# Performance work log

Hardware: AMD Instinct MI355X
Metric: run time of the kernel (lower is better)

Reference implementation:

```python
import jax, jax.numpy as jnp
import numpy as np


def setup_inputs() -> dict:
    key = jax.random.key(0)
    ks = jax.random.split(key, 7)
    B = 65536
    x = jax.random.normal(ks[0], (B, 1, 28, 28), dtype=jnp.float32)
    conv_w = jax.random.normal(ks[1], (4, 1, 7, 7), dtype=jnp.float32) * 0.1
    conv_b = jax.random.normal(ks[2], (4,), dtype=jnp.float32) * 0.1
    fc1_w = jax.random.normal(ks[3], (64, 256), dtype=jnp.float32) * 0.05
    fc1_b = jax.random.normal(ks[4], (64,), dtype=jnp.float32) * 0.05
    fc2_w = jax.random.normal(ks[5], (10, 64), dtype=jnp.float32) * 0.1
    fc2_b = jax.random.normal(ks[6], (10,), dtype=jnp.float32) * 0.1
    return {"x": x, "conv_w": conv_w, "conv_b": conv_b,
            "fc1_w": fc1_w, "fc1_b": fc1_b, "fc2_w": fc2_w, "fc2_b": fc2_b}


def reference(x, conv_w, conv_b, fc1_w, fc1_b, fc2_w, fc2_b):
    # conv1: 1->4 channels, 7x7 kernel, stride 3, no padding -> [B,4,8,8]
    h = jax.lax.conv_general_dilated(
        x, conv_w, window_strides=(3, 3), padding="VALID",
        dimension_numbers=("NCHW", "OIHW", "NCHW"))
    h = h + conv_b[None, :, None, None]
    h = h * h  # SquareFunction (CKKS polynomial activation)
    h = h.reshape(h.shape[0], -1)  # [B, 256]
    h = jnp.einsum("bi,oi->bo", h, fc1_w) + fc1_b
    h = h * h  # SquareFunction
    out = jnp.einsum("bi,oi->bo", h, fc2_w) + fc2_b  # [B, 10]
    return out
```

## Files before the change

### kernel.cpp

```cpp
#include <hip/hip_runtime.h>


#define BLK_IMGS    32
#define CHUNK_IMGS  8
#define NCHUNK      4
#define XCH_FLOATS  (CHUNK_IMGS * 784)
#define HB_PITCH    33
#define H2_PITCH    33

#define LDS_XBUF    0
#define LDS_H       6272
#define LDS_H2      14720
#define LDS_W2      16832
#define LDS_OUT     17856
#define LDS_TOTAL_F 18176

__global__ __launch_bounds__(512)
void encconv_fused8(const float* __restrict__ x,
                    const float* __restrict__ conv_w,
                    const float* __restrict__ conv_b,
                    const float* __restrict__ fc1_w,
                    const float* __restrict__ fc1_b,
                    const float* __restrict__ fc2_w,
                    const float* __restrict__ fc2_b,
                    float* __restrict__ out)
{
    extern __shared__ float lds[];
    float*  xbuf = lds + LDS_XBUF;
    float4* hb   = (float4*)(lds + LDS_H);
    float4* h2b  = (float4*)(lds + LDS_H2);
    float4* w2b  = (float4*)(lds + LDS_W2);
    float*  ob   = lds + LDS_OUT;

    const int tid  = threadIdx.x;
    const int blk  = blockIdx.x;
    const long base_img = (long)blk * BLK_IMGS;

    const int lane = tid & 63;
    const int wv   = tid >> 6;

    const int c    = __builtin_amdgcn_readfirstlane(wv >> 1);
    const int ghi  = __builtin_amdgcn_readfirstlane(wv & 1);
    const int glo  = lane >> 4;
    const int y    = (lane >> 1) & 7;
    const int xh   = lane & 1;
    const int g    = ghi * 4 + glo;

    float ws[49];
    #pragma unroll
    for (int i = 0; i < 49; ++i) ws[i] = conv_w[c * 49 + i];
    const float cb = conv_b[c];

    if (tid < 160) {
        float4 v = *(const float4*)(fc2_w + tid * 4);
        int e  = tid * 4;
        int j  = e >> 6;
        int kk = (e & 63) >> 2;
        w2b[kk * 16 + j] = v;
    }

    const float* xblk = x + base_img * 784;

    float4 pf0, pf1, pf2, pf3;
    {
        const float* src = xblk;
        pf0 = *(const float4*)(src + 4 * tid);
        pf1 = *(const float4*)(src + 4 * (tid + 512));
        pf2 = *(const float4*)(src + 4 * (tid + 1024));
        if (tid < 32) pf3 = *(const float4*)(src + 4 * (tid + 1536));
    }

    for (int ch = 0; ch < NCHUNK; ++ch) {
        *(float4*)(xbuf + 4 * tid)          = pf0;
        *(float4*)(xbuf + 4 * (tid + 512))  = pf1;
        *(float4*)(xbuf + 4 * (tid + 1024)) = pf2;
        if (tid < 32) *(float4*)(xbuf + 4 * (tid + 1536)) = pf3;
        __syncthreads();

        if (ch + 1 < NCHUNK) {
            const float* src = xblk + (ch + 1) * XCH_FLOATS;
            pf0 = *(const float4*)(src + 4 * tid);
            pf1 = *(const float4*)(src + 4 * (tid + 512));
            pf2 = *(const float4*)(src + 4 * (tid + 1024));
            if (tid < 32) pf3 = *(const float4*)(src + 4 * (tid + 1536));
        }

        float acc0 = 0.f, acc1 = 0.f, acc2 = 0.f, acc3 = 0.f;
        const float* xi = xbuf + g * 784;
        #pragma unroll
        for (int rr = 0; rr < 7; ++rr) {
            const float* rp = xi + (3 * y + rr) * 28 + 12 * xh;
            float4 r0 = *(const float4*)(rp + 0);
            float4 r1 = *(const float4*)(rp + 4);
            float4 r2 = *(const float4*)(rp + 8);
            float4 r3 = *(const float4*)(rp + 12);
            float r[16] = { r0.x, r0.y, r0.z, r0.w,
                            r1.x, r1.y, r1.z, r1.w,
                            r2.x, r2.y, r2.z, r2.w,
                            r3.x, r3.y, r3.z, r3.w };
            #pragma unroll
            for (int kx = 0; kx < 7; ++kx) {
                const float w = ws[rr * 7 + kx];
                acc0 = fmaf(r[0 + kx], w, acc0);
                acc1 = fmaf(r[3 + kx], w, acc1);
                acc2 = fmaf(r[6 + kx], w, acc2);
                acc3 = fmaf(r[9 + kx], w, acc3);
            }
        }

        float4 hv;
        hv.x = acc0 + cb; hv.x *= hv.x;
        hv.y = acc1 + cb; hv.y *= hv.y;
        hv.z = acc2 + cb; hv.z *= hv.z;
        hv.w = acc3 + cb; hv.w *= hv.w;
        hb[(c * 16 + y * 2 + xh) * HB_PITCH + (ch * CHUNK_IMGS + g)] = hv;

        __syncthreads();
    }

    {
        const int img = lane & 31;
        const int oh  = lane >> 5;
        const int w8  = __builtin_amdgcn_readfirstlane(wv);
        const float* wbase = fc1_w + (w8 * 8) * 256;

        float a0=0.f,a1=0.f,a2=0.f,a3=0.f,a4=0.f,a5=0.f,a6=0.f,a7=0.f;

        #pragma unroll 2
        for (int k4 = 0; k4 < 64; ++k4) {
            float4 h4 = hb[k4 * HB_PITCH + img];
            const float* wp = wbase + k4 * 4;
            float4 w0 = *(const float4*)(wp + 0 * 256);
            float4 w1 = *(const float4*)(wp + 1 * 256);
            float4 w2 = *(const float4*)(wp + 2 * 256);
            float4 w3 = *(const float4*)(wp + 3 * 256);
            float4 w4 = *(const float4*)(wp + 4 * 256);
            float4 w5 = *(const float4*)(wp + 5 * 256);
            float4 w6 = *(const float4*)(wp + 6 * 256);
            float4 w7 = *(const float4*)(wp + 7 * 256);
            a0 = fmaf(h4.x,w0.x,a0); a0 = fmaf(h4.y,w0.y,a0); a0 = fmaf(h4.z,w0.z,a0); a0 = fmaf(h4.w,w0.w,a0);
            a1 = fmaf(h4.x,w1.x,a1); a1 = fmaf(h4.y,w1.y,a1); a1 = fmaf(h4.z,w1.z,a1); a1 = fmaf(h4.w,w1.w,a1);
            a2 = fmaf(h4.x,w2.x,a2); a2 = fmaf(h4.y,w2.y,a2); a2 = fmaf(h4.z,w2.z,a2); a2 = fmaf(h4.w,w2.w,a2);
            a3 = fmaf(h4.x,w3.x,a3); a3 = fmaf(h4.y,w3.y,a3); a3 = fmaf(h4.z,w3.z,a3); a3 = fmaf(h4.w,w3.w,a3);
            a4 = fmaf(h4.x,w4.x,a4); a4 = fmaf(h4.y,w4.y,a4); a4 = fmaf(h4.z,w4.z,a4); a4 = fmaf(h4.w,w4.w,a4);
            a5 = fmaf(h4.x,w5.x,a5); a5 = fmaf(h4.y,w5.y,a5); a5 = fmaf(h4.z,w5.z,a5); a5 = fmaf(h4.w,w5.w,a5);
            a6 = fmaf(h4.x,w6.x,a6); a6 = fmaf(h4.y,w6.y,a6); a6 = fmaf(h4.z,w6.z,a6); a6 = fmaf(h4.w,w6.w,a6);
            a7 = fmaf(h4.x,w7.x,a7); a7 = fmaf(h4.y,w7.y,a7); a7 = fmaf(h4.z,w7.z,a7); a7 = fmaf(h4.w,w7.w,a7);
        }

        const float* bp = fc1_b + w8 * 8;
        float s0 = oh ? a4 : a0;  float b0 = oh ? bp[4] : bp[0];
        float s1 = oh ? a5 : a1;  float b1 = oh ? bp[5] : bp[1];
        float s2 = oh ? a6 : a2;  float b2 = oh ? bp[6] : bp[2];
        float s3 = oh ? a7 : a3;  float b3 = oh ? bp[7] : bp[3];
        float4 p0;
        p0.x = s0 + b0; p0.x *= p0.x;
        p0.y = s1 + b1; p0.y *= p0.y;
        p0.z = s2 + b2; p0.z *= p0.z;
        p0.w = s3 + b3; p0.w *= p0.w;
        h2b[(w8 * 2 + oh) * H2_PITCH + img] = p0;
    }
    __syncthreads();

    {
        const int im5 = tid >> 4;
        const int q   = tid & 15;
        if (q < 10) {
            float s = 0.f;
            #pragma unroll
            for (int k4 = 0; k4 < 16; ++k4) {
                float4 hh = h2b[k4 * H2_PITCH + im5];
                float4 wA = w2b[k4 * 16 + q];
                s = fmaf(hh.x, wA.x, s); s = fmaf(hh.y, wA.y, s);
                s = fmaf(hh.z, wA.z, s); s = fmaf(hh.w, wA.w, s);
            }
            ob[im5 * 10 + q] = s + fc2_b[q];
        }
    }
    __syncthreads();

    if (tid < 80) {
        float4 v = *(const float4*)(ob + tid * 4);
        *(float4*)(out + (long)blk * 320 + tid * 4) = v;
    }
}

extern "C" void kernel_launch(void* const* d_in, const int* in_sizes, int n_in,
                              void* d_out, int out_size, void* d_ws, size_t ws_size,
                              hipStream_t stream) {
    const float* x      = (const float*)d_in[0];
    const float* conv_w = (const float*)d_in[1];
    const float* conv_b = (const float*)d_in[2];
    const float* fc1_w  = (const float*)d_in[3];
    const float* fc1_b  = (const float*)d_in[4];
    const float* fc2_w  = (const float*)d_in[5];
    const float* fc2_b  = (const float*)d_in[6];
    float* out = (float*)d_out;

    const int B = in_sizes[0] / 784;
    const int blocks = (B + BLK_IMGS - 1) / BLK_IMGS;
    const size_t lds_bytes = LDS_TOTAL_F * sizeof(float);

    static bool attr_set = false;
    if (!attr_set) {
        (void)hipFuncSetAttribute((const void*)encconv_fused8,
                                  hipFuncAttributeMaxDynamicSharedMemorySize,
                                  (int)lds_bytes);
        attr_set = true;
    }

    encconv_fused8<<<blocks, 512, lds_bytes, stream>>>(
        x, conv_w, conv_b, fc1_w, fc1_b, fc2_w, fc2_b, out);
}
```

Baseline: 344.2 us.

## Halve conv chunk size and alias LDS buffers to shrink footprint

```diff
diff --git a/kernel.cpp b/kernel.cpp
--- a/kernel.cpp
+++ b/kernel.cpp
@@ -2,21 +2,19 @@
 
 
 #define BLK_IMGS    32
-#define CHUNK_IMGS  8
-#define NCHUNK      4
+#define CHUNK_IMGS  4
+#define NCHUNK      8
 #define XCH_FLOATS  (CHUNK_IMGS * 784)
 #define HB_PITCH    33
 #define H2_PITCH    33
 
 #define LDS_XBUF    0
-#define LDS_H       6272
-#define LDS_H2      14720
-#define LDS_W2      16832
-#define LDS_OUT     17856
-#define LDS_TOTAL_F 18176
+#define LDS_H       3136
+#define LDS_W2      11584
+#define LDS_TOTAL_F 12608
 
 __global__ __launch_bounds__(512)
-void encconv_fused8(const float* __restrict__ x,
+void encconv_fused9(const float* __restrict__ x,
                     const float* __restrict__ conv_w,
                     const float* __restrict__ conv_b,
                     const float* __restrict__ fc1_w,
@@ -27,10 +25,11 @@
 {
     extern __shared__ float lds[];
     float*  xbuf = lds + LDS_XBUF;
-    float4* hb   = (float4*)(lds + LDS_H);
-    float4* h2b  = (float4*)(lds + LDS_H2);
+    float*  hbf  = lds + LDS_H;
+    float4* hb   = (float4*)hbf;
+    float4* h2b  = (float4*)(lds + LDS_XBUF);
+    float*  ob   = lds + LDS_XBUF + 2112;
     float4* w2b  = (float4*)(lds + LDS_W2);
-    float*  ob   = lds + LDS_OUT;
 
     const int tid  = threadIdx.x;
     const int blk  = blockIdx.x;
@@ -40,11 +39,13 @@
     const int wv   = tid >> 6;
 
     const int c    = __builtin_amdgcn_readfirstlane(wv >> 1);
-    const int ghi  = __builtin_amdgcn_readfirstlane(wv & 1);
-    const int glo  = lane >> 4;
-    const int y    = (lane >> 1) & 7;
-    const int xh   = lane & 1;
-    const int g    = ghi * 4 + glo;
+    const int gh   = __builtin_amdgcn_readfirstlane(wv & 1);
+    const int gl   = lane >> 5;
+    const int y    = (lane >> 2) & 7;
+    const int xq   = lane & 3;
+    const int g    = gh * 2 + gl;
+    const int x0   = xq & 1;
+    const int xh2  = xq >> 1;
 
     float ws[49];
     #pragma unroll
@@ -61,59 +62,49 @@
 
     const float* xblk = x + base_img * 784;
 
-    float4 pf0, pf1, pf2, pf3;
+    float4 pf0, pf1;
     {
-        const float* src = xblk;
-        pf0 = *(const float4*)(src + 4 * tid);
-        pf1 = *(const float4*)(src + 4 * (tid + 512));
-        pf2 = *(const float4*)(src + 4 * (tid + 1024));
-        if (tid < 32) pf3 = *(const float4*)(src + 4 * (tid + 1536));
+        pf0 = *(const float4*)(xblk + 4 * tid);
+        if (tid < 272) pf1 = *(const float4*)(xblk + 4 * (tid + 512));
     }
 
     for (int ch = 0; ch < NCHUNK; ++ch) {
-        *(float4*)(xbuf + 4 * tid)          = pf0;
-        *(float4*)(xbuf + 4 * (tid + 512))  = pf1;
-        *(float4*)(xbuf + 4 * (tid + 1024)) = pf2;
-        if (tid < 32) *(float4*)(xbuf + 4 * (tid + 1536)) = pf3;
+        *(float4*)(xbuf + 4 * tid) = pf0;
+        if (tid < 272) *(float4*)(xbuf + 4 * (tid + 512)) = pf1;
         __syncthreads();
 
         if (ch + 1 < NCHUNK) {
             const float* src = xblk + (ch + 1) * XCH_FLOATS;
             pf0 = *(const float4*)(src + 4 * tid);
-            pf1 = *(const float4*)(src + 4 * (tid + 512));
-            pf2 = *(const float4*)(src + 4 * (tid + 1024));
-            if (tid < 32) pf3 = *(const float4*)(src + 4 * (tid + 1536));
+            if (tid < 272) pf1 = *(const float4*)(src + 4 * (tid + 512));
         }
 
-        float acc0 = 0.f, acc1 = 0.f, acc2 = 0.f, acc3 = 0.f;
+        float acc0 = 0.f, acc1 = 0.f;
         const float* xi = xbuf + g * 784;
         #pragma unroll
         for (int rr = 0; rr < 7; ++rr) {
-            const float* rp = xi + (3 * y + rr) * 28 + 12 * xh;
-            float4 r0 = *(const float4*)(rp + 0);
-            float4 r1 = *(const float4*)(rp + 4);
-            float4 r2 = *(const float4*)(rp + 8);
-            float4 r3 = *(const float4*)(rp + 12);
-            float r[16] = { r0.x, r0.y, r0.z, r0.w,
-                            r1.x, r1.y, r1.z, r1.w,
-                            r2.x, r2.y, r2.z, r2.w,
-                            r3.x, r3.y, r3.z, r3.w };
+            const float* rp = xi + (3 * y + rr) * 28 + 6 * xq;
+            float2 q0 = *(const float2*)(rp + 0);
+            float2 q1 = *(const float2*)(rp + 2);
+            float2 q2 = *(const float2*)(rp + 4);
+            float2 q3 = *(const float2*)(rp + 6);
+            float2 q4 = *(const float2*)(rp + 8);
+            float r[10] = { q0.x, q0.y, q1.x, q1.y, q2.x,
+                            q2.y, q3.x, q3.y, q4.x, q4.y };
             #pragma unroll
             for (int kx = 0; kx < 7; ++kx) {
                 const float w = ws[rr * 7 + kx];
                 acc0 = fmaf(r[0 + kx], w, acc0);
                 acc1 = fmaf(r[3 + kx], w, acc1);
-                acc2 = fmaf(r[6 + kx], w, acc2);
-                acc3 = fmaf(r[9 + kx], w, acc3);
             }
         }
 
-        float4 hv;
-        hv.x = acc0 + cb; hv.x *= hv.x;
-        hv.y = acc1 + cb; hv.y *= hv.y;
-        hv.z = acc2 + cb; hv.z *= hv.z;
-        hv.w = acc3 + cb; hv.w *= hv.w;
-        hb[(c * 16 + y * 2 + xh) * HB_PITCH + (ch * CHUNK_IMGS + g)] = hv;
+        float h0 = acc0 + cb; h0 *= h0;
+        float h1 = acc1 + cb; h1 *= h1;
+        const int k4  = c * 16 + y * 2 + xh2;
+        const int img = ch * CHUNK_IMGS + g;
+        float2 hv2; hv2.x = h0; hv2.y = h1;
+        *(float2*)(hbf + (k4 * HB_PITCH + img) * 4 + 2 * x0) = hv2;
 
         __syncthreads();
     }
@@ -201,14 +192,6 @@
     const int blocks = (B + BLK_IMGS - 1) / BLK_IMGS;
     const size_t lds_bytes = LDS_TOTAL_F * sizeof(float);
 
-    static bool attr_set = false;
-    if (!attr_set) {
-        (void)hipFuncSetAttribute((const void*)encconv_fused8,
-                                  hipFuncAttributeMaxDynamicSharedMemorySize,
-                                  (int)lds_bytes);
-        attr_set = true;
-    }
-
-    encconv_fused8<<<blocks, 512, lds_bytes, stream>>>(
+    encconv_fused9<<<blocks, 512, lds_bytes, stream>>>(
         x, conv_w, conv_b, fc1_w, fc1_b, fc2_w, fc2_b, out);
 }
```

Result: faster. 334.2 us (-2.9%).
